# Performance work log

Measured on AMD Instinct MI355X. Metric: run time of the kernel, lower is better.

The kernel has to match this reference:

```python
import jax, jax.numpy as jnp
import numpy as np

B, N, D, C, NCLS = 8, 2048, 256, 128, 50
EPS = 1e-5  # BatchNorm eps

def _bn(x, g, b):
    # eval-mode BatchNorm1d over channel dim of (B,C,N): running_mean=0, running_var=1
    return x * (g / jnp.sqrt(1.0 + EPS))[:, None] + b[:, None]

def _complex_linear(x, Wr, br, Wi, bi):
    # torch ComplexLinear: complex(fr(x.real)-fi(x.imag), fr(x.imag)+fi(x.real))
    xr, xi = x.real, x.imag
    re = (xr @ Wr.T + br) - (xi @ Wi.T + bi)
    im = (xi @ Wr.T + br) + (xr @ Wi.T + bi)
    return jax.lax.complex(re, im)

def _sa(x, qkW, vW, vb, tW, tb, g, b):
    # x: (B,C,N); q/k share weights (tied in torch), dim C//4
    xq = jnp.einsum('qc,bcn->bnq', qkW, x)            # (B,N,C/4)
    xk = jnp.einsum('qc,bcm->bqm', qkW, x)            # (B,C/4,N)
    energy = jnp.einsum('bnq,bqm->bnm', xq, xk)       # (B,N,N)
    attn = jax.nn.softmax(energy, axis=-1)
    attn = attn / (1e-9 + attn.sum(axis=1, keepdims=True))  # column renorm
    xv = jnp.einsum('oc,bcn->bon', vW, x) + vb[:, None]
    xr = x - jnp.einsum('bcn,bnm->bcm', xv, attn)
    xr = jnp.einsum('oc,bcn->bon', tW, xr) + tb[:, None]
    return x + jax.nn.relu(_bn(xr, g, b))

def reference(xyz, cls_label, A, Bmat, W1r, b1r, W1i, b1i, W2r, b2r, W2i, b2i,
              lbl_emb, ft_w1, ft_g1, ft_b1, ft_w2, ft_g2, ft_b2,
              sa_qk, sa_vw, sa_vb, sa_tw, sa_tb, sa_g, sa_b,
              fuse_w, fuse_g, fuse_b, c1_w, c1_b, bn1_g, bn1_b, c2_w, c2_b):
    pts = xyz.transpose(0, 2, 1)                       # (B,N,3)
    # VecKM(d=256, alpha=30, beta=9): G = eB (eB^H eA), normalized to sqrt(d)
    eA = jnp.exp(1j * (pts @ A))                       # (B,N,D) complex64
    eB = jnp.exp(1j * (pts @ Bmat))
    inner = jnp.einsum('bnd,bne->bde', eB.conj(), eA)  # (B,D,D)
    G = jnp.einsum('bnd,bde->bne', eB, inner)          # (B,N,D)
    G = G / jnp.linalg.norm(G, axis=-1, keepdims=True) * jnp.sqrt(jnp.float32(D))
    G = _complex_linear(G, W1r, b1r, W1i, b1i)
    G = jax.lax.complex(jax.nn.relu(G.real), jax.nn.relu(G.imag))  # ComplexReLU
    G = _complex_linear(G, W2r, b2r, W2i, b2i)
    G = (G.real ** 2 + G.imag ** 2).transpose(0, 2, 1)  # (B,D,N)
    reweight = (cls_label @ lbl_emb)[:, :, None]        # (B,D,1)
    x = G * reweight
    x = jax.nn.relu(_bn(jnp.einsum('oc,bcn->bon', ft_w1, x), ft_g1, ft_b1))
    x = _bn(jnp.einsum('oc,bcn->bon', ft_w2, x), ft_g2, ft_b2)  # (B,C,N)
    feats = []
    for i in range(4):
        x = _sa(x, sa_qk[i], sa_vw[i], sa_vb[i], sa_tw[i], sa_tb[i], sa_g[i], sa_b[i])
        feats.append(x)
    x = jnp.concatenate(feats, axis=1)                  # (B,4C,N)
    x = jax.nn.relu(_bn(jnp.einsum('oc,bcn->bon', fuse_w, x), fuse_g, fuse_b))
    x = jax.nn.relu(_bn(jnp.einsum('oc,bcn->bon', c1_w, x) + c1_b[:, None], bn1_g, bn1_b))
    # dropout is identity in eval mode
    x = jnp.einsum('oc,bcn->bon', c2_w, x) + c2_b[:, None]
    x = jax.nn.log_softmax(x, axis=1)
    return x.transpose(0, 2, 1)                         # (B,N,NCLS)

def setup_inputs():
    key = jax.random.key(0)
    k = jax.random.split(key, 24)
    rn = lambda i, s: jax.random.normal(k[i], s, jnp.float32)
    s = 0.05
    return {
        'xyz': rn(0, (B, 3, N)),
        'cls_label': jax.random.uniform(k[1], (B, 16), jnp.float32),
        'A': rn(2, (3, D)) * 30.0,
        'Bmat': rn(3, (3, D)) * 9.0,
        'W1r': rn(4, (D, D)) * s, 'b1r': rn(5, (D,)) * s,
        'W1i': rn(6, (D, D)) * s, 'b1i': rn(7, (D,)) * s,
        'W2r': rn(8, (D, D)) * s, 'b2r': rn(9, (D,)) * s,
        'W2i': rn(10, (D, D)) * s, 'b2i': rn(11, (D,)) * s,
        'lbl_emb': rn(12, (16, D)),
        'ft_w1': rn(13, (C, D)) * s, 'ft_g1': jnp.ones((C,)), 'ft_b1': jnp.zeros((C,)),
        'ft_w2': rn(14, (C, C)) * s, 'ft_g2': jnp.ones((C,)), 'ft_b2': jnp.zeros((C,)),
        'sa_qk': rn(15, (4, C // 4, C)) * s,
        'sa_vw': rn(16, (4, C, C)) * s, 'sa_vb': rn(17, (4, C)) * s,
        'sa_tw': rn(18, (4, C, C)) * s, 'sa_tb': rn(19, (4, C)) * s,
        'sa_g': jnp.ones((4, C)), 'sa_b': jnp.zeros((4, C)),
        'fuse_w': rn(20, (C, 4 * C)) * s, 'fuse_g': jnp.ones((C,)), 'fuse_b': jnp.zeros((C,)),
        'c1_w': rn(21, (C, C)) * s, 'c1_b': rn(22, (C,)) * s,
        'bn1_g': jnp.ones((C,)), 'bn1_b': jnp.zeros((C,)),
        'c2_w': rn(23, (NCLS, C)) * s, 'c2_b': jnp.zeros((NCLS,)),
    }
```

## Files before the change

### kernel.cpp

```cpp
#include <hip/hip_runtime.h>

#define BB 8
#define NPTS 2048
#define DD 256
#define CCH 128
#define NCLASS 50
#define LOG2E 1.4426950408889634f

typedef __attribute__((ext_vector_type(8))) short short8;
typedef __attribute__((ext_vector_type(4))) float f32x4;
typedef unsigned short u16;
#define MFMA16(a,b,c) __builtin_amdgcn_mfma_f32_16x16x32_bf16(a,b,c,0,0,0)

__device__ __forceinline__ u16 f2bf(float x){
  union { float f; unsigned int u; } v; v.f = x;
  unsigned int r = v.u + 0x7FFFu + ((v.u >> 16) & 1u);
  return (u16)(r >> 16);
}
__device__ __forceinline__ float bf2f(u16 u){
  union { unsigned int u32; float f; } v; v.u32 = ((unsigned int)u) << 16; return v.f;
}
__device__ __forceinline__ void split2(float x, u16& h, u16& l){
  h = f2bf(x); l = f2bf(x - bf2f(h));
}
// ... 231 lines not shown
  for (int rg = 0; rg < 2; rg++) {
    ar_[rg] = (size_t)(m0 + wr + rg*16 + r16)*DD + g4*8;
    br_[rg] = (size_t)(o0 + wc + rg*16 + r16)*DD + g4*8;
  }
  #pragma unroll
  for (int k0 = 0; k0 < DD; k0 += 32) {
    short8 arh[2], arl[2], aih[2], ail[2], brh[2], brl[2], bih[2], bil[2];
    #pragma unroll
    for (int rg = 0; rg < 2; rg++) {
      arh[rg] = ld8(Arh + ar_[rg] + k0); arl[rg] = ld8(Arl + ar_[rg] + k0);
      aih[rg] = ld8(Aih + ar_[rg] + k0); ail[rg] = ld8(Ail + ar_[rg] + k0);
      brh[rg] = ld8(Wrh + br_[rg] + k0); brl[rg] = ld8(Wrl + br_[rg] + k0);
      bih[rg] = ld8(Wih + br_[rg] + k0); bil[rg] = ld8(Wil + br_[rg] + k0);
    }
    #pragma unroll
    for (int ra = 0; ra < 2; ra++)
      #pragma unroll
      for (int rb = 0; rb < 2; rb++) {
        p[ra][rb] = MFMA16(arh[ra], brh[rb], p[ra][rb]);
        p[ra][rb] = MFMA16(arh[ra], brl[rb], p[ra][rb]);
        p[ra][rb] = MFMA16(arl[ra], brh[rb], p[ra][rb]);
        q[ra][rb] = MFMA16(aih[ra], bih[rb], q[ra][rb]);
        q[ra][rb] = MFMA16(aih[ra], bil[rb], q[ra][rb]);
        q[ra][rb] = MFMA16(ail[ra], bih[rb], q[ra][rb]);
        im[ra][rb] = MFMA16(arh[ra], bih[rb], im[ra][rb]);
        im[ra][rb] = MFMA16(arh[ra], bil[rb], im[ra][rb]);
        im[ra][rb] = MFMA16(arl[ra], bih[rb], im[ra][rb]);
        im[ra][rb] = MFMA16(aih[ra], brh[rb], im[ra][rb]);
        im[ra][rb] = MFMA16(aih[ra], brl[rb], im[ra][rb]);
        im[ra][rb] = MFMA16(ail[ra], brh[rb], im[ra][rb]);
      }
  }
  #pragma unroll
  for (int ra = 0; ra < 2; ra++)
    #pragma unroll
    for (int rb = 0; rb < 2; rb++) {
      int o = o0 + wc + rb*16 + r16;
      float brv = br[o], biv = bi[o];
      if (mode == 1) {
        #pragma unroll
        for (int j = 0; j < 4; j++) {
          int m = m0 + wr + ra*16 + g4*4 + j;
          float re = fmaxf(p[ra][rb][j] - q[ra][rb][j] + brv - biv, 0.f);
          float iv = fmaxf(im[ra][rb][j] + brv + biv, 0.f);
          size_t off = (size_t)m*DD + o;
          u16 h, l;
          split2(re, h, l); Orh[off] = h; Orl[off] = l;
          split2(iv, h, l); Oih[off] = h; Oil[off] = l;
        }
      } else {
        int mbase = m0 + wr + ra*16 + g4*4;
        int b = mbase >> 11, nb = mbase & (NPTS-1);
        float rwv = RW[(size_t)b*DD + o];
        float4 gv;
        #pragma unroll
        for (int j = 0; j < 4; j++) {
          float re = p[ra][rb][j] - q[ra][rb][j] + brv - biv;
          float iv = im[ra][rb][j] + brv + biv;
          ((float*)&gv)[j] = (re*re + iv*iv) * rwv;
        }
        *(float4*)(GSQ + ((size_t)b*DD + o)*NPTS + nb) = gv;
      }
    }
}

__global__ void rw_kernel(const float* __restrict__ cls, const float* __restrict__ lbl,
                          float* __restrict__ RW)
{
  int b = blockIdx.x; int d = threadIdx.x;
  float s = 0.f;
  #pragma unroll
  for (int k = 0; k < 16; k++) s += cls[b*16+k] * lbl[k*DD+d];
  RW[b*DD+d] = s;
}

__global__ __launch_bounds__(256) void sgemm_kernel(
    const u16* __restrict__ Wh, const u16* __restrict__ Wl,
    const float* __restrict__ X, float* __restrict__ Y,
    const float* __restrict__ RES,
    const float* __restrict__ bias, const float* __restrict__ bng, const float* __restrict__ bnb,
    u16* __restrict__ YBh, u16* __restrict__ YBl, int ybmode,
    int O, int Cin, size_t xbs, size_t ybs, size_t rbs, int flags)
{
  int b = blockIdx.z;
  int n0 = blockIdx.x*64, o0 = blockIdx.y*64;
  const float* x = X + (size_t)b*xbs;
  __shared__ u16 sXh[64][40], sXl[64][40];
  int tid = threadIdx.x, lane = tid & 63, w = tid >> 6;
  int wo = (w >> 1)*32, wn = (w & 1)*32;
  int r16 = lane & 15, g4 = lane >> 4;
  f32x4 acc[2][2] = {};
  int stc = tid >> 3;
  int stn = (tid & 7)*8;
  for (int k0 = 0; k0 < Cin; k0 += 32) {
    const float* px = x + (size_t)(k0+stc)*NPTS + n0 + stn;
    float4 u0 = *(const float4*)px;
    float4 u1 = *(const float4*)(px+4);
    float v[8] = {u0.x,u0.y,u0.z,u0.w,u1.x,u1.y,u1.z,u1.w};
    __syncthreads();
    #pragma unroll
    for (int j = 0; j < 8; j++) {
      u16 h, l; split2(v[j], h, l);
      sXh[stn+j][stc] = h; sXl[stn+j][stc] = l;
    }
    __syncthreads();
    short8 awh[2], awl[2], bxh[2], bxl[2];
    #pragma unroll
    for (int rg = 0; rg < 2; rg++) {
      int orow = o0 + wo + rg*16 + r16;
      if (orow < O) {
        size_t woff = (size_t)orow*Cin + k0 + g4*8;
        awh[rg] = ld8(Wh + woff); awl[rg] = ld8(Wl + woff);
      } else { awh[rg] = zero8(); awl[rg] = zero8(); }
      bxh[rg] = ld8(&sXh[wn + rg*16 + r16][g4*8]);
      bxl[rg] = ld8(&sXl[wn + rg*16 + r16][g4*8]);
    }
    #pragma unroll
    for (int ra = 0; ra < 2; ra++)
      #pragma unroll
      for (int rb = 0; rb < 2; rb++) {
        acc[ra][rb] = MFMA16(awh[ra], bxh[rb], acc[ra][rb]);
        acc[ra][rb] = MFMA16(awh[ra], bxl[rb], acc[ra][rb]);
        acc[ra][rb] = MFMA16(awl[ra], bxh[rb], acc[ra][rb]);
      }
  }
  #pragma unroll
  for (int ra = 0; ra < 2; ra++)
    #pragma unroll
    for (int rb = 0; rb < 2; rb++)
      #pragma unroll
      for (int j = 0; j < 4; j++) {
        int o = o0 + wo + ra*16 + g4*4 + j;
        if (o >= O) continue;
        int n = n0 + wn + rb*16 + r16;
        float v = acc[ra][rb][j];
        if (flags & 1) v += bias[o];
        if (flags & 2) v = v * (bng[o] * rsqrtf(1.f + 1e-5f)) + bnb[o];
        if (flags & 4) v = fmaxf(v, 0.f);
        if (flags & 8) v += RES[(size_t)b*rbs + (size_t)o*NPTS + n];
        if (ybmode == 0) Y[(size_t)b*ybs + (size_t)o*NPTS + n] = v;
        else if (ybmode == 1) YBh[(size_t)b*ybs + (size_t)o*NPTS + n] = f2bf(v);
        else {
          u16 h, l; split2(v, h, l);
          size_t off = ((size_t)b*NPTS + n)*32 + o;
          YBh[off] = h; YBl[off] = l;
        }
      }
}

__global__ __launch_bounds__(256) void sastat_kernel(
    const u16* __restrict__ Qh, const u16* __restrict__ Ql,
    float* __restrict__ PM, float* __restrict__ PS)
{
  int b = blockIdx.z, ch = blockIdx.y;
  int n0 = blockIdx.x*64;
  size_t base = (size_t)b*NPTS*32;
  int tid = threadIdx.x, lane = tid & 63, wid = tid >> 6;
  int r16 = lane & 15, g4 = lane >> 4;
  size_t ao = base + (size_t)(n0 + wid*16 + r16)*32 + g4*8;
  short8 ah = ld8(Qh + ao), al = ld8(Ql + ao);
  float pm[4] = {-3.4e38f,-3.4e38f,-3.4e38f,-3.4e38f};
  float ps[4] = {0.f,0.f,0.f,0.f};
  int mbeg = ch*512, mend = mbeg + 512;
  for (int mt = mbeg; mt < mend; mt += 32) {
    size_t bo0 = base + (size_t)(mt + r16)*32 + g4*8;
    size_t bo1 = bo0 + 16*32;
    short8 bh0 = ld8(Qh+bo0), bl0 = ld8(Ql+bo0);
    short8 bh1 = ld8(Qh+bo1), bl1 = ld8(Ql+bo1);
    f32x4 a0 = {}, a1 = {};
    a0 = MFMA16(ah, bh0, a0); a0 = MFMA16(ah, bl0, a0); a0 = MFMA16(al, bh0, a0);
    a1 = MFMA16(ah, bh1, a1); a1 = MFMA16(ah, bl1, a1); a1 = MFMA16(al, bh1, a1);
    #pragma unroll
    for (int j = 0; j < 4; j++) {
      float v = fmaxf(a0[j], a1[j]);
      float mn = fmaxf(pm[j], v);
      ps[j] = ps[j]*exp2f((pm[j]-mn)*LOG2E)
            + exp2f((a0[j]-mn)*LOG2E) + exp2f((a1[j]-mn)*LOG2E);
      pm[j] = mn;
    }
  }
  #pragma unroll
  for (int j = 0; j < 4; j++) {
    float m = pm[j], s = ps[j];
    #pragma unroll
    for (int d = 1; d < 16; d <<= 1) {
      float om = __shfl_xor(m, d);
      float os = __shfl_xor(s, d);
      float mn = fmaxf(m, om);
      s = s*exp2f((m-mn)*LOG2E) + os*exp2f((om-mn)*LOG2E);
      m = mn;
    }
    if (r16 == 0) {
      int n_ = n0 + wid*16 + g4*4 + j;
      size_t off = ((size_t)ch*BB + b)*NPTS + n_;
      PM[off] = m; PS[off] = s;
    }
  }
}

__global__ __launch_bounds__(256) void comb1_kernel(
    const float* __restrict__ PM, const float* __restrict__ PS,
    float* __restrict__ MX, float* __restrict__ RS)
{
  size_t i = (size_t)blockIdx.x*256 + threadIdx.x;
  const size_t S = (size_t)BB*NPTS;
  float m0 = PM[i], m1 = PM[i+S], m2 = PM[i+2*S], m3 = PM[i+3*S];
  float mx = fmaxf(fmaxf(m0,m1), fmaxf(m2,m3));
  float den = PS[i]*exp2f((m0-mx)*LOG2E) + PS[i+S]*exp2f((m1-mx)*LOG2E)
            + PS[i+2*S]*exp2f((m2-mx)*LOG2E) + PS[i+3*S]*exp2f((m3-mx)*LOG2E);
  MX[i] = mx; RS[i] = 1.f/den;
}

__global__ __launch_bounds__(256) void fused_pv_kernel(
    const u16* __restrict__ Qh, const u16* __restrict__ Ql,
    const float* __restrict__ MX, const float* __restrict__ RS,
    const u16* __restrict__ XV, const float* __restrict__ XRES, size_t res_bs,
    float* __restrict__ OUT)
{
  int b = blockIdx.y;
  int m0 = blockIdx.x*16;
  size_t qbase = (size_t)b*NPTS*32;
  const u16* xv = XV + (size_t)b*CCH*NPTS;
  const float* mx = MX + (size_t)b*NPTS;
  const float* rs = RS + (size_t)b*NPTS;
  __shared__ u16 Pl[2][16][72];
  __shared__ float csacc[16];
  int tid = threadIdx.x, lane = tid & 63, w = tid >> 6;
  int r16 = lane & 15, g4 = lane >> 4;
  if (tid < 16) csacc[tid] = 0.f;
  int nb = w;
  int cw = w*32;
  int nloc = nb*16 + g4*4;
  size_t mo = qbase + (size_t)(m0 + r16)*32 + g4*8;
  short8 mbh = ld8(Qh + mo), mbl = ld8(Ql + mo);
  const u16* pa0 = xv + (size_t)(cw + r16)*NPTS + g4*8;
  const u16* pa1 = pa0 + (size_t)16*NPTS;
  f32x4 acc[2] = {};
  float csl = 0.f;

  #define COMPUTE_P(NT, BUF) { \
    size_t no_ = qbase + (size_t)((NT) + nb*16 + r16)*32 + g4*8; \
    short8 nah = ld8(Qh + no_), nal = ld8(Ql + no_); \
    f32x4 e = {}; \
    e = MFMA16(nah, mbh, e); e = MFMA16(nah, mbl, e); e = MFMA16(nal, mbh, e); \
    float4 mx4 = *(const float4*)&mx[(NT) + nloc]; \
    float4 rs4 = *(const float4*)&rs[(NT) + nloc]; \
    float t0 = exp2f((e[0]-mx4.x)*LOG2E)*rs4.x; \
    float t1 = exp2f((e[1]-mx4.y)*LOG2E)*rs4.y; \
    float t2 = exp2f((e[2]-mx4.z)*LOG2E)*rs4.z; \
    float t3 = exp2f((e[3]-mx4.w)*LOG2E)*rs4.w; \
    csl += t0 + t1 + t2 + t3; \
    uint2 pk; \
    pk.x = (unsigned)f2bf(t0) | ((unsigned)f2bf(t1) << 16); \
    pk.y = (unsigned)f2bf(t2) | ((unsigned)f2bf(t3) << 16); \
    *(uint2*)&Pl[BUF][r16][nloc] = pk; }

  COMPUTE_P(0, 0);
  __syncthreads();
  int cur = 0;
  for (int nt = 0; nt < NPTS; nt += 64) {
    short8 xa0 = ld8(pa0 + nt), xa1 = ld8(pa1 + nt);
    short8 xb0 = ld8(pa0 + nt + 32), xb1 = ld8(pa1 + nt + 32);
    short8 p0  = *(const short8*)&Pl[cur][r16][g4*8];
    short8 p0b = *(const short8*)&Pl[cur][r16][32 + g4*8];
    if (nt + 64 < NPTS) { COMPUTE_P(nt + 64, cur ^ 1); }
    acc[0] = MFMA16(xa0, p0, acc[0]);
    acc[1] = MFMA16(xa1, p0, acc[1]);
    acc[0] = MFMA16(xb0, p0b, acc[0]);
    acc[1] = MFMA16(xb1, p0b, acc[1]);
    __syncthreads();
    cur ^= 1;
  }
  #undef COMPUTE_P
  {
    float c = csl;
    c += __shfl_xor(c, 16);
    c += __shfl_xor(c, 32);
    if (g4 == 0) atomicAdd(&csacc[r16], c);
  }
  __syncthreads();
  float ci = 1.f/(1e-9f + csacc[r16]);
  int m = m0 + r16;
  #pragma unroll
  for (int ca = 0; ca < 2; ca++)
    #pragma unroll
    for (int j = 0; j < 4; j++) {
      int c = cw + ca*16 + g4*4 + j;
      float v = XRES[(size_t)b*res_bs + (size_t)c*NPTS + m] - acc[ca][j]*ci;
      OUT[((size_t)b*CCH + c)*NPTS + m] = v;
    }
}

__global__ __launch_bounds__(256) void lsm_kernel(const float* __restrict__ Y,
                                                  float* __restrict__ OUT)
{
  int idx = blockIdx.x*256 + threadIdx.x;
  int b = idx >> 11, n = idx & (NPTS-1);
  const float* p = Y + (size_t)b*NCLASS*NPTS + n;
  float m = -3.4e38f;
  #pragma unroll
  for (int k = 0; k < NCLASS; k++) m = fmaxf(m, p[(size_t)k*NPTS]);
  float s = 0.f;
  #pragma unroll
  for (int k = 0; k < NCLASS; k++) s += expf(p[(size_t)k*NPTS] - m);
  float L = m + logf(s);
  float* o = OUT + (size_t)idx*NCLASS;
  #pragma unroll
  for (int k = 0; k < NCLASS; k++) o[k] = p[(size_t)k*NPTS] - L;
}

extern "C" void kernel_launch(void* const* d_in, const int* in_sizes, int n_in,
                              void* d_out, int out_size, void* d_ws, size_t ws_size,
                              hipStream_t stream)
{
  (void)in_sizes; (void)n_in; (void)out_size; (void)ws_size;
  const float* xyz  = (const float*)d_in[0];
  const float* cls  = (const float*)d_in[1];
  const float* Amat = (const float*)d_in[2];
  const float* Bm   = (const float*)d_in[3];
  const float* W1r  = (const float*)d_in[4];
  const float* b1r  = (const float*)d_in[5];
  const float* W1i  = (const float*)d_in[6];
  const float* b1i  = (const float*)d_in[7];
  const float* W2r  = (const float*)d_in[8];
  const float* b2r  = (const float*)d_in[9];
  const float* W2i  = (const float*)d_in[10];
  const float* b2i  = (const float*)d_in[11];
  const float* lbl  = (const float*)d_in[12];
  const float* ftw1 = (const float*)d_in[13];
  const float* ftg1 = (const float*)d_in[14];
  const float* ftb1 = (const float*)d_in[15];
  const float* ftw2 = (const float*)d_in[16];
  const float* ftg2 = (const float*)d_in[17];
  const float* ftb2 = (const float*)d_in[18];
  const float* saqk = (const float*)d_in[19];
  const float* savw = (const float*)d_in[20];
  const float* savb = (const float*)d_in[21];
  const float* satw = (const float*)d_in[22];
  const float* satb = (const float*)d_in[23];
  const float* sag  = (const float*)d_in[24];
  const float* sab  = (const float*)d_in[25];
  const float* fusew= (const float*)d_in[26];
  const float* fuseg= (const float*)d_in[27];
  const float* fuseb= (const float*)d_in[28];
  const float* c1w  = (const float*)d_in[29];
  const float* c1b  = (const float*)d_in[30];
  const float* bn1g = (const float*)d_in[31];
  const float* bn1b = (const float*)d_in[32];
  const float* c2w  = (const float*)d_in[33];
  const float* c2b  = (const float*)d_in[34];
  float* out = (float*)d_out;

  float* ws = (float*)d_ws;
  const size_t PS  = (size_t)BB*DD*NPTS;
  const size_t ISZ = (size_t)BB*DD*DD;
  u16* U = (u16*)ws;
  u16 *ATrh = U+0*PS, *ATrl = U+1*PS, *ATih = U+2*PS, *ATil = U+3*PS;
  u16 *BTrh = U+4*PS, *BTrl = U+5*PS, *BTih = U+6*PS, *BTil = U+7*PS;
  u16 *Bnrh = U+8*PS, *Bnrl = U+9*PS, *Bnih = U+10*PS, *Bnil = U+11*PS;
  u16 *Irh = U+12*PS, *Irl = U+12*PS+ISZ, *Iih = U+12*PS+2*ISZ, *Iil = U+12*PS+3*ISZ;
  float* gsq = (float*)(U + 12*PS + 4*ISZ);
  float2* PART = (float2*)gsq;
  float2* Gf = (float2*)ws;
  u16 *G1rh = U+4*PS, *G1rl = U+5*PS, *G1ih = U+6*PS, *G1il = U+7*PS;
  u16 *G2rh = U+8*PS, *G2rl = U+9*PS, *G2ih = U+10*PS, *G2il = U+11*PS;
  size_t p = (size_t)BB*NPTS*NPTS;
  float* xfeat = ws + p;  p += (size_t)BB*CCH*NPTS;
  float* feats = ws + p;  p += (size_t)BB*4*CCH*NPTS;
  float* xt1   = ws + p;  p += (size_t)BB*CCH*NPTS;
  float* xt2   = ws + p;  p += (size_t)BB*CCH*NPTS;
  float* ybuf  = ws + p;  p += (size_t)BB*NCLASS*NPTS;
  float* rwb   = ws + p;  p += (size_t)BB*DD;
  float* mxv   = ws + p;  p += (size_t)BB*NPTS;
  float* rsv   = ws + p;  p += (size_t)BB*NPTS;
  float* PMb   = ws + p;  p += (size_t)4*BB*NPTS;
  float* PSb   = ws + p;  p += (size_t)4*BB*NPTS;
  u16* xqh = (u16*)(ws + p);
  u16* xql = xqh + (size_t)BB*NPTS*32;
  u16* xvb = xql + (size_t)BB*NPTS*32;
  u16* wpH = xvb + (size_t)BB*CCH*NPTS;
  u16* wpL = wpH + 557056;

  const int o_w1r=0, o_w1i=65536, o_w2r=131072, o_w2i=196608, o_ft1=262144,
            o_ft2=294912, o_qk=311296, o_vw=327680, o_tw=393216, o_fu=458752,
            o_c1=524288, o_c2=540672;
  WSplit wsp;
  const float* srcs[12] = {W1r,W1i,W2r,W2i,ftw1,ftw2,saqk,savw,satw,fusew,c1w,c2w};
  const int cnts[12] = {65536,65536,65536,65536,32768,16384,16384,65536,65536,65536,16384,6400};
  const int offs[12] = {o_w1r,o_w1i,o_w2r,o_w2i,o_ft1,o_ft2,o_qk,o_vw,o_tw,o_fu,o_c1,o_c2};
  for (int i = 0; i < 12; i++) { wsp.src[i]=srcs[i]; wsp.cnt[i]=cnts[i]; wsp.off[i]=offs[i]; }

  wsplit_kernel<<<dim3(256, 12), 256, 0, stream>>>(wsp, wpH, wpL);
  rw_kernel<<<BB, DD, 0, stream>>>(cls, lbl, rwb);
  ek1_kernel<<<(int)(PS/256), 256, 0, stream>>>(xyz, Amat, Bm,
      ATrh, ATrl, ATih, ATil, BTrh, BTrl, BTih, BTil);
  ek2_kernel<<<(int)(PS/256), 256, 0, stream>>>(xyz, Bm, Bnrh, Bnrl, Bnih, Bnil);
  inner_mfma_kernel<<<dim3(DD/64, DD/64, BB*4), 256, 0, stream>>>(
      ATrh, ATrl, ATih, ATil, BTrh, BTrl, BTih, BTil, PART);
  innred_kernel<<<(int)(ISZ/256), 256, 0, stream>>>(PART, Irh, Irl, Iih, Iil);
  g_mfma_kernel<<<dim3(DD/64, NPTS/64, BB), 256, 0, stream>>>(
      Bnrh, Bnrl, Bnih, Bnil, Irh, Irl, Iih, Iil, Gf);
  gnormsplit_kernel<<<BB*NPTS, 256, 0, stream>>>(Gf, G1rh, G1rl, G1ih, G1il);
  clinear_mfma_kernel<<<dim3(DD/64, (BB*NPTS)/64), 256, 0, stream>>>(
      G1rh, G1rl, G1ih, G1il, wpH+o_w1r, wpL+o_w1r, wpH+o_w1i, wpL+o_w1i,
      b1r, b1i, G2rh, G2rl, G2ih, G2il, nullptr, nullptr, 1);
  clinear_mfma_kernel<<<dim3(DD/64, (BB*NPTS)/64), 256, 0, stream>>>(
      G2rh, G2rl, G2ih, G2il, wpH+o_w2r, wpL+o_w2r, wpH+o_w2i, wpL+o_w2i,
      b2r, b2i, nullptr, nullptr, nullptr, nullptr, rwb, gsq, 2);

  sgemm_kernel<<<dim3(NPTS/64, CCH/64, BB), 256, 0, stream>>>(
      wpH+o_ft1, wpL+o_ft1, gsq, xt1, nullptr, nullptr, ftg1, ftb1, nullptr, nullptr, 0,
      CCH, DD, (size_t)DD*NPTS, (size_t)CCH*NPTS, 0, 2|4);
  sgemm_kernel<<<dim3(NPTS/64, CCH/64, BB), 256, 0, stream>>>(
      wpH+o_ft2, wpL+o_ft2, xt1, xfeat, nullptr, nullptr, ftg2, ftb2, nullptr, nullptr, 0,
      CCH, CCH, (size_t)CCH*NPTS, (size_t)CCH*NPTS, 0, 2);

  const float* xsrc = xfeat;
  size_t xbs = (size_t)CCH*NPTS;
  for (int i = 0; i < 4; i++) {
    sgemm_kernel<<<dim3(NPTS/64, 1, BB), 256, 0, stream>>>(
        wpH+o_qk + i*32*CCH, wpL+o_qk + i*32*CCH, xsrc, nullptr, nullptr,
        nullptr, nullptr, nullptr, xqh, xql, 2, 32, CCH, xbs, 0, 0, 0);
    sastat_kernel<<<dim3(NPTS/64, 4, BB), 256, 0, stream>>>(xqh, xql, PMb, PSb);
    comb1_kernel<<<(BB*NPTS)/256, 256, 0, stream>>>(PMb, PSb, mxv, rsv);
    sgemm_kernel<<<dim3(NPTS/64, CCH/64, BB), 256, 0, stream>>>(
        wpH+o_vw + i*CCH*CCH, wpL+o_vw + i*CCH*CCH, xsrc, nullptr, nullptr,
        savb + i*CCH, nullptr, nullptr, xvb, nullptr, 1, CCH, CCH, xbs,
        (size_t)CCH*NPTS, 0, 1);
    fused_pv_kernel<<<dim3(NPTS/16, BB), 256, 0, stream>>>(
        xqh, xql, mxv, rsv, xvb, xsrc, xbs, xt2);
    sgemm_kernel<<<dim3(NPTS/64, CCH/64, BB), 256, 0, stream>>>(
        wpH+o_tw + i*CCH*CCH, wpL+o_tw + i*CCH*CCH, xt2, feats + (size_t)i*CCH*NPTS, xsrc,
        satb + i*CCH, sag + i*CCH, sab + i*CCH, nullptr, nullptr, 0,
        CCH, CCH, (size_t)CCH*NPTS, (size_t)4*CCH*NPTS, xbs, 1|2|4|8);
    xsrc = feats + (size_t)i*CCH*NPTS;
    xbs = (size_t)4*CCH*NPTS;
  }

  sgemm_kernel<<<dim3(NPTS/64, CCH/64, BB), 256, 0, stream>>>(
      wpH+o_fu, wpL+o_fu, feats, xt1, nullptr, nullptr, fuseg, fuseb, nullptr, nullptr, 0,
      CCH, 4*CCH, (size_t)4*CCH*NPTS, (size_t)CCH*NPTS, 0, 2|4);
  sgemm_kernel<<<dim3(NPTS/64, CCH/64, BB), 256, 0, stream>>>(
      wpH+o_c1, wpL+o_c1, xt1, xt2, nullptr, c1b, bn1g, bn1b, nullptr, nullptr, 0,
      CCH, CCH, (size_t)CCH*NPTS, (size_t)CCH*NPTS, 0, 1|2|4);
  sgemm_kernel<<<dim3(NPTS/64, 1, BB), 256, 0, stream>>>(
      wpH+o_c2, wpL+o_c2, xt2, ybuf, nullptr, c2b, nullptr, nullptr, nullptr, nullptr, 0,
      NCLASS, CCH, (size_t)CCH*NPTS, (size_t)NCLASS*NPTS, 0, 1);
  lsm_kernel<<<(BB*NPTS)/256, 256, 0, stream>>>(ybuf, out);
}
```

Before: 997.1 us.

## Software-prefetch Q and XV loads and swizzle P tile in fused PV kernel

Register-prefetches the Q hi/lo fragments two tiles ahead and the XV fragments one tile ahead, so global load latency overlaps the MFMA and exp work of the current tile. It also replaces the padded shared-memory P buffer with an XOR-swizzled layout to avoid bank conflicts without padding. The cost is higher register pressure, which may reduce occupancy, plus extra index arithmetic.

```diff
diff --git a/kernel.cpp b/kernel.cpp
--- a/kernel.cpp
+++ b/kernel.cpp
@@ -478,26 +478,29 @@
   const u16* xv = XV + (size_t)b*CCH*NPTS;
   const float* mx = MX + (size_t)b*NPTS;
   const float* rs = RS + (size_t)b*NPTS;
-  __shared__ u16 Pl[2][16][72];
+  __shared__ u16 Pl[2][16*64];
   __shared__ float csacc[16];
   int tid = threadIdx.x, lane = tid & 63, w = tid >> 6;
   int r16 = lane & 15, g4 = lane >> 4;
   if (tid < 16) csacc[tid] = 0.f;
   int nb = w;
   int cw = w*32;
+  int swz = (r16 & 7) << 3;
   int nloc = nb*16 + g4*4;
+  int wrc = r16*64 + (nloc ^ swz);
+  int rd0 = r16*64 + ((g4*8) ^ swz);
+  int rd1 = r16*64 + ((32 + g4*8) ^ swz);
   size_t mo = qbase + (size_t)(m0 + r16)*32 + g4*8;
   short8 mbh = ld8(Qh + mo), mbl = ld8(Ql + mo);
   const u16* pa0 = xv + (size_t)(cw + r16)*NPTS + g4*8;
   const u16* pa1 = pa0 + (size_t)16*NPTS;
+  size_t q0 = qbase + (size_t)(nb*16 + r16)*32 + g4*8;
   f32x4 acc[2] = {};
   float csl = 0.f;
 
-  #define COMPUTE_P(NT, BUF) { \
-    size_t no_ = qbase + (size_t)((NT) + nb*16 + r16)*32 + g4*8; \
-    short8 nah = ld8(Qh + no_), nal = ld8(Ql + no_); \
+  #define COMPUTE_P(NT, QH, QL, BUF) { \
     f32x4 e = {}; \
-    e = MFMA16(nah, mbh, e); e = MFMA16(nah, mbl, e); e = MFMA16(nal, mbh, e); \
+    e = MFMA16(QH, mbh, e); e = MFMA16(QH, mbl, e); e = MFMA16(QL, mbh, e); \
     float4 mx4 = *(const float4*)&mx[(NT) + nloc]; \
     float4 rs4 = *(const float4*)&rs[(NT) + nloc]; \
     float t0 = exp2f((e[0]-mx4.x)*LOG2E)*rs4.x; \
@@ -508,22 +511,36 @@
     uint2 pk; \
     pk.x = (unsigned)f2bf(t0) | ((unsigned)f2bf(t1) << 16); \
     pk.y = (unsigned)f2bf(t2) | ((unsigned)f2bf(t3) << 16); \
-    *(uint2*)&Pl[BUF][r16][nloc] = pk; }
-
-  COMPUTE_P(0, 0);
+    *(uint2*)&Pl[BUF][wrc] = pk; }
+
+  short8 qh_c = ld8(Qh + q0), ql_c = ld8(Ql + q0);
+  short8 qh_n = ld8(Qh + q0 + (size_t)64*32), ql_n = ld8(Ql + q0 + (size_t)64*32);
+  short8 xa0 = ld8(pa0), xa1 = ld8(pa1);
+  short8 xb0 = ld8(pa0 + 32), xb1 = ld8(pa1 + 32);
+  COMPUTE_P(0, qh_c, ql_c, 0);
   __syncthreads();
   int cur = 0;
   for (int nt = 0; nt < NPTS; nt += 64) {
-    short8 xa0 = ld8(pa0 + nt), xa1 = ld8(pa1 + nt);
-    short8 xb0 = ld8(pa0 + nt + 32), xb1 = ld8(pa1 + nt + 32);
-    short8 p0  = *(const short8*)&Pl[cur][r16][g4*8];
-    short8 p0b = *(const short8*)&Pl[cur][r16][32 + g4*8];
-    if (nt + 64 < NPTS) { COMPUTE_P(nt + 64, cur ^ 1); }
+    short8 qh_2 = qh_n, ql_2 = ql_n;
+    short8 xn0 = xa0, xn1 = xa1, xn2 = xb0, xn3 = xb1;
+    if (nt + 128 < NPTS) {
+      size_t qo = q0 + (size_t)(nt + 128)*32;
+      qh_2 = ld8(Qh + qo); ql_2 = ld8(Ql + qo);
+    }
+    if (nt + 64 < NPTS) {
+      xn0 = ld8(pa0 + nt + 64); xn1 = ld8(pa1 + nt + 64);
+      xn2 = ld8(pa0 + nt + 96); xn3 = ld8(pa1 + nt + 96);
+    }
+    short8 p0  = ld8(&Pl[cur][rd0]);
+    short8 p0b = ld8(&Pl[cur][rd1]);
+    if (nt + 64 < NPTS) { COMPUTE_P(nt + 64, qh_n, ql_n, cur ^ 1); }
     acc[0] = MFMA16(xa0, p0, acc[0]);
     acc[1] = MFMA16(xa1, p0, acc[1]);
     acc[0] = MFMA16(xb0, p0b, acc[0]);
     acc[1] = MFMA16(xb1, p0b, acc[1]);
     __syncthreads();
+    qh_n = qh_2; ql_n = ql_2;
+    xa0 = xn0; xa1 = xn1; xb0 = xn2; xb1 = xn3;
     cur ^= 1;
   }
   #undef COMPUTE_P
```

Result: no change. 996.4 us (-0.1%).

## Enlarge fused attention-PV tile to 64 query columns with 8 waves and prefetch

Applied to the files above, without the earlier changes.

The fused softmax-times-V kernel now handles 64 output columns per block with 512 threads, where it previously handled 16 with 256. Each wave computes a 16x32 energy slab and reuses each loaded V fragment across four column sub-tiles, so V is read from global memory a quarter as often and the P tile is shared by more waves. The P tile in shared memory uses an XOR swizzle to avoid bank conflicts, and Q and V fragments are register-prefetched two iterations ahead. In exchange the kernel uses more registers and launches fewer blocks, which could lower occupancy.

```diff
diff --git a/kernel.cpp b/kernel.cpp
--- a/kernel.cpp
+++ b/kernel.cpp
@@ -466,64 +466,101 @@
   MX[i] = mx; RS[i] = 1.f/den;
 }
 
-__global__ __launch_bounds__(256) void fused_pv_kernel(
+__global__ __launch_bounds__(512) void fused_pv_kernel(
     const u16* __restrict__ Qh, const u16* __restrict__ Ql,
     const float* __restrict__ MX, const float* __restrict__ RS,
     const u16* __restrict__ XV, const float* __restrict__ XRES, size_t res_bs,
     float* __restrict__ OUT)
 {
   int b = blockIdx.y;
-  int m0 = blockIdx.x*16;
+  int m0 = blockIdx.x*64;
   size_t qbase = (size_t)b*NPTS*32;
   const u16* xv = XV + (size_t)b*CCH*NPTS;
   const float* mx = MX + (size_t)b*NPTS;
   const float* rs = RS + (size_t)b*NPTS;
-  __shared__ u16 Pl[2][16][72];
-  __shared__ float csacc[16];
+  __shared__ u16 Pl[2][64*66];
+  __shared__ float csacc[64];
   int tid = threadIdx.x, lane = tid & 63, w = tid >> 6;
   int r16 = lane & 15, g4 = lane >> 4;
-  if (tid < 16) csacc[tid] = 0.f;
-  int nb = w;
-  int cw = w*32;
-  int nloc = nb*16 + g4*4;
-  size_t mo = qbase + (size_t)(m0 + r16)*32 + g4*8;
+  if (tid < 64) csacc[tid] = 0.f;
+  int ma = w >> 1, na = w & 1;
+  int cw = w*16;
+  int swz = (r16 & 7) << 3;
+  size_t mo = qbase + (size_t)(m0 + ma*16 + r16)*32 + g4*8;
   short8 mbh = ld8(Qh + mo), mbl = ld8(Ql + mo);
-  const u16* pa0 = xv + (size_t)(cw + r16)*NPTS + g4*8;
-  const u16* pa1 = pa0 + (size_t)16*NPTS;
-  f32x4 acc[2] = {};
+  int wr_base = (ma*16 + r16)*66;
+  int nl0 = na*32 + g4*4;
+  const u16* pa = xv + (size_t)(cw + r16)*NPTS + g4*8;
+  size_t qn_off = qbase + (size_t)(na*32 + r16)*32 + g4*8;
+  f32x4 acc[4] = {};
   float csl = 0.f;
 
-  #define COMPUTE_P(NT, BUF) { \
-    size_t no_ = qbase + (size_t)((NT) + nb*16 + r16)*32 + g4*8; \
-    short8 nah = ld8(Qh + no_), nal = ld8(Ql + no_); \
-    f32x4 e = {}; \
-    e = MFMA16(nah, mbh, e); e = MFMA16(nah, mbl, e); e = MFMA16(nal, mbh, e); \
-    float4 mx4 = *(const float4*)&mx[(NT) + nloc]; \
-    float4 rs4 = *(const float4*)&rs[(NT) + nloc]; \
-    float t0 = exp2f((e[0]-mx4.x)*LOG2E)*rs4.x; \
-    float t1 = exp2f((e[1]-mx4.y)*LOG2E)*rs4.y; \
-    float t2 = exp2f((e[2]-mx4.z)*LOG2E)*rs4.z; \
-    float t3 = exp2f((e[3]-mx4.w)*LOG2E)*rs4.w; \
-    csl += t0 + t1 + t2 + t3; \
-    uint2 pk; \
-    pk.x = (unsigned)f2bf(t0) | ((unsigned)f2bf(t1) << 16); \
-    pk.y = (unsigned)f2bf(t2) | ((unsigned)f2bf(t3) << 16); \
-    *(uint2*)&Pl[BUF][r16][nloc] = pk; }
-
-  COMPUTE_P(0, 0);
+  #define COMPUTE_P(NT, QH0, QL0, QH1, QL1, BUF) { \
+    f32x4 e0 = {}, e1 = {}; \
+    e0 = MFMA16(QH0, mbh, e0); e0 = MFMA16(QH0, mbl, e0); e0 = MFMA16(QL0, mbh, e0); \
+    e1 = MFMA16(QH1, mbh, e1); e1 = MFMA16(QH1, mbl, e1); e1 = MFMA16(QL1, mbh, e1); \
+    { float4 m4 = *(const float4*)&mx[(NT) + nl0]; \
+      float4 r4 = *(const float4*)&rs[(NT) + nl0]; \
+      float t0 = exp2f((e0[0]-m4.x)*LOG2E)*r4.x; \
+      float t1 = exp2f((e0[1]-m4.y)*LOG2E)*r4.y; \
+      float t2 = exp2f((e0[2]-m4.z)*LOG2E)*r4.z; \
+      float t3 = exp2f((e0[3]-m4.w)*LOG2E)*r4.w; \
+      csl += t0 + t1 + t2 + t3; \
+      uint2 pk; \
+      pk.x = (unsigned)f2bf(t0) | ((unsigned)f2bf(t1) << 16); \
+      pk.y = (unsigned)f2bf(t2) | ((unsigned)f2bf(t3) << 16); \
+      *(uint2*)&Pl[BUF][wr_base + (nl0 ^ swz)] = pk; } \
+    { float4 m4 = *(const float4*)&mx[(NT) + nl0 + 16]; \
+      float4 r4 = *(const float4*)&rs[(NT) + nl0 + 16]; \
+      float t0 = exp2f((e1[0]-m4.x)*LOG2E)*r4.x; \
+      float t1 = exp2f((e1[1]-m4.y)*LOG2E)*r4.y; \
+      float t2 = exp2f((e1[2]-m4.z)*LOG2E)*r4.z; \
+      float t3 = exp2f((e1[3]-m4.w)*LOG2E)*r4.w; \
+      csl += t0 + t1 + t2 + t3; \
+      uint2 pk; \
+      pk.x = (unsigned)f2bf(t0) | ((unsigned)f2bf(t1) << 16); \
+      pk.y = (unsigned)f2bf(t2) | ((unsigned)f2bf(t3) << 16); \
+      *(uint2*)&Pl[BUF][wr_base + ((nl0 + 16) ^ swz)] = pk; } }
+
+  short8 qch[2], qcl[2], qnh[2], qnl[2];
+  #pragma unroll
+  for (int s = 0; s < 2; s++) {
+    size_t o = qn_off + (size_t)(s*16)*32;
+    qch[s] = ld8(Qh + o); qcl[s] = ld8(Ql + o);
+    o += (size_t)64*32;
+    qnh[s] = ld8(Qh + o); qnl[s] = ld8(Ql + o);
+  }
+  short8 xa0 = ld8(pa), xa1 = ld8(pa + 32);
+  short8 xn0 = ld8(pa + 64), xn1 = ld8(pa + 96);
+  COMPUTE_P(0, qch[0], qcl[0], qch[1], qcl[1], 0);
   __syncthreads();
   int cur = 0;
   for (int nt = 0; nt < NPTS; nt += 64) {
-    short8 xa0 = ld8(pa0 + nt), xa1 = ld8(pa1 + nt);
-    short8 xb0 = ld8(pa0 + nt + 32), xb1 = ld8(pa1 + nt + 32);
-    short8 p0  = *(const short8*)&Pl[cur][r16][g4*8];
-    short8 p0b = *(const short8*)&Pl[cur][r16][32 + g4*8];
-    if (nt + 64 < NPTS) { COMPUTE_P(nt + 64, cur ^ 1); }
-    acc[0] = MFMA16(xa0, p0, acc[0]);
-    acc[1] = MFMA16(xa1, p0, acc[1]);
-    acc[0] = MFMA16(xb0, p0b, acc[0]);
-    acc[1] = MFMA16(xb1, p0b, acc[1]);
+    short8 q2h[2], q2l[2], x20, x21;
+    if (nt + 128 < NPTS) {
+      #pragma unroll
+      for (int s = 0; s < 2; s++) {
+        size_t o = qn_off + (size_t)(nt + 128 + s*16)*32;
+        q2h[s] = ld8(Qh + o); q2l[s] = ld8(Ql + o);
+      }
+      x20 = ld8(pa + nt + 128); x21 = ld8(pa + nt + 160);
+    } else { q2h[0]=q2h[1]=q2l[0]=q2l[1]=x20=x21=zero8(); }
+    short8 pf0[4], pf1[4];
+    #pragma unroll
+    for (int mf = 0; mf < 4; mf++) {
+      int rowb = (mf*16 + r16)*66;
+      pf0[mf] = ld8(&Pl[cur][rowb + ((g4*8) ^ swz)]);
+      pf1[mf] = ld8(&Pl[cur][rowb + ((32 + g4*8) ^ swz)]);
+    }
+    if (nt + 64 < NPTS) { COMPUTE_P(nt + 64, qnh[0], qnl[0], qnh[1], qnl[1], cur ^ 1); }
+    #pragma unroll
+    for (int mf = 0; mf < 4; mf++) {
+      acc[mf] = MFMA16(xa0, pf0[mf], acc[mf]);
+      acc[mf] = MFMA16(xa1, pf1[mf], acc[mf]);
+    }
     __syncthreads();
+    qnh[0]=q2h[0]; qnh[1]=q2h[1]; qnl[0]=q2l[0]; qnl[1]=q2l[1];
+    xa0 = xn0; xa1 = xn1; xn0 = x20; xn1 = x21;
     cur ^= 1;
   }
   #undef COMPUTE_P
@@ -531,19 +568,20 @@
     float c = csl;
     c += __shfl_xor(c, 16);
     c += __shfl_xor(c, 32);
-    if (g4 == 0) atomicAdd(&csacc[r16], c);
+    if (g4 == 0) atomicAdd(&csacc[ma*16 + r16], c);
   }
   __syncthreads();
-  float ci = 1.f/(1e-9f + csacc[r16]);
-  int m = m0 + r16;
-  #pragma unroll
-  for (int ca = 0; ca < 2; ca++)
+  #pragma unroll
+  for (int mf = 0; mf < 4; mf++) {
+    int m = m0 + mf*16 + r16;
+    float ci = 1.f/(1e-9f + csacc[mf*16 + r16]);
     #pragma unroll
     for (int j = 0; j < 4; j++) {
-      int c = cw + ca*16 + g4*4 + j;
-      float v = XRES[(size_t)b*res_bs + (size_t)c*NPTS + m] - acc[ca][j]*ci;
+      int c = cw + g4*4 + j;
+      float v = XRES[(size_t)b*res_bs + (size_t)c*NPTS + m] - acc[mf][j]*ci;
       OUT[((size_t)b*CCH + c)*NPTS + m] = v;
     }
+  }
 }
 
 __global__ __launch_bounds__(256) void lsm_kernel(const float* __restrict__ Y,
@@ -682,7 +720,7 @@
         wpH+o_vw + i*CCH*CCH, wpL+o_vw + i*CCH*CCH, xsrc, nullptr, nullptr,
         savb + i*CCH, nullptr, nullptr, xvb, nullptr, 1, CCH, CCH, xbs,
         (size_t)CCH*NPTS, 0, 1);
-    fused_pv_kernel<<<dim3(NPTS/16, BB), 256, 0, stream>>>(
+    fused_pv_kernel<<<dim3(NPTS/64, BB), 512, 0, stream>>>(
         xqh, xql, mxv, rsv, xvb, xsrc, xbs, xt2);
     sgemm_kernel<<<dim3(NPTS/64, CCH/64, BB), 256, 0, stream>>>(
         wpH+o_tw + i*CCH*CCH, wpL+o_tw + i*CCH*CCH, xt2, feats + (size_t)i*CCH*NPTS, xsrc,
```

After: 962.2 us. 1.04x faster.

## Split attention PV over key chunks with per-wave register P and combine kernel

Applied to the files above, without the earlier changes.

Rewrites the fused attention-times-value kernel so each wave owns 16 query columns and one quarter of the key range. The P tile is redistributed through lane shuffles instead of a double-buffered LDS tile, which removes the per-iteration block barrier. Partial accumulators and column sums are written to workspace and reduced by a new sacomb kernel that applies the renormalisation and residual through an LDS transpose. Block indices in both attention kernels are linearised with batch innermost. This buys more parallelism and no barriers at the cost of extra global traffic for partials and one more launch.

```diff
diff --git a/kernel.cpp b/kernel.cpp
--- a/kernel.cpp
+++ b/kernel.cpp
@@ -407,8 +407,11 @@
     const u16* __restrict__ Qh, const u16* __restrict__ Ql,
     float* __restrict__ PM, float* __restrict__ PS)
 {
-  int b = blockIdx.z, ch = blockIdx.y;
-  int n0 = blockIdx.x*64;
+  int bx = blockIdx.x;
+  int b = bx & 7;
+  int t = bx >> 3;
+  int ch = t & 3;
+  int n0 = (t >> 2)*64;
   size_t base = (size_t)b*NPTS*32;
   int tid = threadIdx.x, lane = tid & 63, wid = tid >> 6;
   int r16 = lane & 15, g4 = lane >> 4;
@@ -469,81 +472,126 @@
 __global__ __launch_bounds__(256) void fused_pv_kernel(
     const u16* __restrict__ Qh, const u16* __restrict__ Ql,
     const float* __restrict__ MX, const float* __restrict__ RS,
-    const u16* __restrict__ XV, const float* __restrict__ XRES, size_t res_bs,
-    float* __restrict__ OUT)
-{
-  int b = blockIdx.y;
-  int m0 = blockIdx.x*16;
+    const u16* __restrict__ XV,
+    float* __restrict__ ACCp, float* __restrict__ CSPp)
+{
+  int bx = blockIdx.x;
+  int b = bx & 7;
+  int r = bx >> 3;
+  int ch = r & 3;
+  int mtile = r >> 2;
+  int tid = threadIdx.x, lane = tid & 63, w = tid >> 6;
+  int r16 = lane & 15, g4 = lane >> 4;
+  int m0w = mtile*64 + w*16;
   size_t qbase = (size_t)b*NPTS*32;
   const u16* xv = XV + (size_t)b*CCH*NPTS;
   const float* mx = MX + (size_t)b*NPTS;
   const float* rs = RS + (size_t)b*NPTS;
-  __shared__ u16 Pl[2][16][72];
-  __shared__ float csacc[16];
-  int tid = threadIdx.x, lane = tid & 63, w = tid >> 6;
-  int r16 = lane & 15, g4 = lane >> 4;
-  if (tid < 16) csacc[tid] = 0.f;
-  int nb = w;
-  int cw = w*32;
-  int nloc = nb*16 + g4*4;
-  size_t mo = qbase + (size_t)(m0 + r16)*32 + g4*8;
+  size_t mo = qbase + (size_t)(m0w + r16)*32 + g4*8;
   short8 mbh = ld8(Qh + mo), mbl = ld8(Ql + mo);
-  const u16* pa0 = xv + (size_t)(cw + r16)*NPTS + g4*8;
-  const u16* pa1 = pa0 + (size_t)16*NPTS;
-  f32x4 acc[2] = {};
+  f32x4 acc[8] = {};
   float csl = 0.f;
-
-  #define COMPUTE_P(NT, BUF) { \
-    size_t no_ = qbase + (size_t)((NT) + nb*16 + r16)*32 + g4*8; \
-    short8 nah = ld8(Qh + no_), nal = ld8(Ql + no_); \
-    f32x4 e = {}; \
-    e = MFMA16(nah, mbh, e); e = MFMA16(nah, mbl, e); e = MFMA16(nal, mbh, e); \
-    float4 mx4 = *(const float4*)&mx[(NT) + nloc]; \
-    float4 rs4 = *(const float4*)&rs[(NT) + nloc]; \
-    float t0 = exp2f((e[0]-mx4.x)*LOG2E)*rs4.x; \
-    float t1 = exp2f((e[1]-mx4.y)*LOG2E)*rs4.y; \
-    float t2 = exp2f((e[2]-mx4.z)*LOG2E)*rs4.z; \
-    float t3 = exp2f((e[3]-mx4.w)*LOG2E)*rs4.w; \
-    csl += t0 + t1 + t2 + t3; \
-    uint2 pk; \
-    pk.x = (unsigned)f2bf(t0) | ((unsigned)f2bf(t1) << 16); \
-    pk.y = (unsigned)f2bf(t2) | ((unsigned)f2bf(t3) << 16); \
-    *(uint2*)&Pl[BUF][r16][nloc] = pk; }
-
-  COMPUTE_P(0, 0);
+  int nbeg = ch*512;
+  int sq = (g4 & 1)*32 + r16;
+  const u16* pb_base = xv + (size_t)r16*NPTS + g4*8;
+  for (int it = 0; it < 16; it++) {
+    int nt = nbeg + it*32;
+    f32x4 e0 = {}, e1 = {};
+    {
+      size_t no = qbase + (size_t)(nt + r16)*32 + g4*8;
+      short8 nh = ld8(Qh + no), nl = ld8(Ql + no);
+      e0 = MFMA16(nh, mbh, e0); e0 = MFMA16(nh, mbl, e0); e0 = MFMA16(nl, mbh, e0);
+      no += (size_t)16*32;
+      short8 nh1 = ld8(Qh + no), nl1 = ld8(Ql + no);
+      e1 = MFMA16(nh1, mbh, e1); e1 = MFMA16(nh1, mbl, e1); e1 = MFMA16(nl1, mbh, e1);
+    }
+    unsigned pk00, pk01, pk10, pk11;
+    {
+      float4 m4 = *(const float4*)&mx[nt + 4*g4];
+      float4 r4 = *(const float4*)&rs[nt + 4*g4];
+      float t0 = exp2f((e0[0]-m4.x)*LOG2E)*r4.x;
+      float t1 = exp2f((e0[1]-m4.y)*LOG2E)*r4.y;
+      float t2 = exp2f((e0[2]-m4.z)*LOG2E)*r4.z;
+      float t3 = exp2f((e0[3]-m4.w)*LOG2E)*r4.w;
+      csl += t0+t1+t2+t3;
+      pk00 = (unsigned)f2bf(t0) | ((unsigned)f2bf(t1)<<16);
+      pk01 = (unsigned)f2bf(t2) | ((unsigned)f2bf(t3)<<16);
+      m4 = *(const float4*)&mx[nt + 16 + 4*g4];
+      r4 = *(const float4*)&rs[nt + 16 + 4*g4];
+      t0 = exp2f((e1[0]-m4.x)*LOG2E)*r4.x;
+      t1 = exp2f((e1[1]-m4.y)*LOG2E)*r4.y;
+      t2 = exp2f((e1[2]-m4.z)*LOG2E)*r4.z;
+      t3 = exp2f((e1[3]-m4.w)*LOG2E)*r4.w;
+      csl += t0+t1+t2+t3;
+      pk10 = (unsigned)f2bf(t0) | ((unsigned)f2bf(t1)<<16);
+      pk11 = (unsigned)f2bf(t2) | ((unsigned)f2bf(t3)<<16);
+    }
+    int a00 = __shfl((int)pk00, sq);
+    int a01 = __shfl((int)pk01, sq);
+    int a10 = __shfl((int)pk10, sq);
+    int a11 = __shfl((int)pk11, sq);
+    int b00 = __shfl((int)pk00, sq+16);
+    int b01 = __shfl((int)pk01, sq+16);
+    int b10 = __shfl((int)pk10, sq+16);
+    int b11 = __shfl((int)pk11, sq+16);
+    bool lo = (lane < 32);
+    union { int u[4]; short8 s; } af;
+    af.u[0] = lo ? a00 : a10;
+    af.u[1] = lo ? a01 : a11;
+    af.u[2] = lo ? b00 : b10;
+    af.u[3] = lo ? b01 : b11;
+    const u16* pb = pb_base + nt;
+    #pragma unroll
+    for (int ct = 0; ct < 8; ct++) {
+      short8 bf = ld8(pb + (size_t)(ct*16)*NPTS);
+      acc[ct] = MFMA16(af.s, bf, acc[ct]);
+    }
+  }
+  csl += __shfl_xor(csl, 16);
+  csl += __shfl_xor(csl, 32);
+  size_t pbase = (size_t)(ch*BB + b);
+  if (lane < 16) CSPp[pbase*NPTS + m0w + r16] = csl;
+  #pragma unroll
+  for (int ct = 0; ct < 8; ct++)
+    #pragma unroll
+    for (int j = 0; j < 4; j++)
+      ACCp[(pbase*NPTS + (size_t)(m0w + 4*g4 + j))*CCH + ct*16 + r16] = acc[ct][j];
+}
+
+__global__ __launch_bounds__(256) void sacomb_kernel(
+    const float* __restrict__ ACCp, const float* __restrict__ CSPp,
+    const float* __restrict__ XRES, size_t res_bs, float* __restrict__ OUT)
+{
+  int mt = blockIdx.x;
+  int b = blockIdx.y;
+  int m0 = mt*64;
+  __shared__ float T[128][65];
+  __shared__ float cinv[64];
+  int tid = threadIdx.x;
+  const size_t S = (size_t)BB*NPTS;
+  if (tid < 64) {
+    size_t o = (size_t)b*NPTS + m0 + tid;
+    float c = CSPp[o] + CSPp[S+o] + CSPp[2*S+o] + CSPp[3*S+o];
+    cinv[tid] = 1.f/(1e-9f + c);
+  }
   __syncthreads();
-  int cur = 0;
-  for (int nt = 0; nt < NPTS; nt += 64) {
-    short8 xa0 = ld8(pa0 + nt), xa1 = ld8(pa1 + nt);
-    short8 xb0 = ld8(pa0 + nt + 32), xb1 = ld8(pa1 + nt + 32);
-    short8 p0  = *(const short8*)&Pl[cur][r16][g4*8];
-    short8 p0b = *(const short8*)&Pl[cur][r16][32 + g4*8];
-    if (nt + 64 < NPTS) { COMPUTE_P(nt + 64, cur ^ 1); }
-    acc[0] = MFMA16(xa0, p0, acc[0]);
-    acc[1] = MFMA16(xa1, p0, acc[1]);
-    acc[0] = MFMA16(xb0, p0b, acc[0]);
-    acc[1] = MFMA16(xb1, p0b, acc[1]);
-    __syncthreads();
-    cur ^= 1;
-  }
-  #undef COMPUTE_P
   {
-    float c = csl;
-    c += __shfl_xor(c, 16);
-    c += __shfl_xor(c, 32);
-    if (g4 == 0) atomicAdd(&csacc[r16], c);
+    int c = tid & 127, mh = tid >> 7;
+    const size_t SA = (size_t)BB*NPTS*CCH;
+    for (int ml = mh; ml < 64; ml += 2) {
+      size_t o = ((size_t)b*NPTS + m0 + ml)*CCH + c;
+      float s = ACCp[o] + ACCp[SA+o] + ACCp[2*SA+o] + ACCp[3*SA+o];
+      T[c][ml] = s * cinv[ml];
+    }
   }
   __syncthreads();
-  float ci = 1.f/(1e-9f + csacc[r16]);
-  int m = m0 + r16;
-  #pragma unroll
-  for (int ca = 0; ca < 2; ca++)
-    #pragma unroll
-    for (int j = 0; j < 4; j++) {
-      int c = cw + ca*16 + g4*4 + j;
-      float v = XRES[(size_t)b*res_bs + (size_t)c*NPTS + m] - acc[ca][j]*ci;
-      OUT[((size_t)b*CCH + c)*NPTS + m] = v;
-    }
+  {
+    int m = tid & 63, c4 = tid >> 6;
+    for (int cl = c4; cl < 128; cl += 4) {
+      size_t o = (size_t)b*res_bs + (size_t)cl*NPTS + m0 + m;
+      OUT[((size_t)b*CCH + cl)*NPTS + m0 + m] = XRES[o] - T[cl][m];
+    }
+  }
 }
 
 __global__ __launch_bounds__(256) void lsm_kernel(const float* __restrict__ Y,
@@ -619,6 +667,8 @@
   float2* Gf = (float2*)ws;
   u16 *G1rh = U+4*PS, *G1rl = U+5*PS, *G1ih = U+6*PS, *G1il = U+7*PS;
   u16 *G2rh = U+8*PS, *G2rl = U+9*PS, *G2ih = U+10*PS, *G2il = U+11*PS;
+  float* ACCp = ws;
+  float* CSPp = ws + (size_t)4*BB*NPTS*CCH;
   size_t p = (size_t)BB*NPTS*NPTS;
   float* xfeat = ws + p;  p += (size_t)BB*CCH*NPTS;
   float* feats = ws + p;  p += (size_t)BB*4*CCH*NPTS;
@@ -676,14 +726,16 @@
     sgemm_kernel<<<dim3(NPTS/64, 1, BB), 256, 0, stream>>>(
         wpH+o_qk + i*32*CCH, wpL+o_qk + i*32*CCH, xsrc, nullptr, nullptr,
         nullptr, nullptr, nullptr, xqh, xql, 2, 32, CCH, xbs, 0, 0, 0);
-    sastat_kernel<<<dim3(NPTS/64, 4, BB), 256, 0, stream>>>(xqh, xql, PMb, PSb);
+    sastat_kernel<<<1024, 256, 0, stream>>>(xqh, xql, PMb, PSb);
     comb1_kernel<<<(BB*NPTS)/256, 256, 0, stream>>>(PMb, PSb, mxv, rsv);
     sgemm_kernel<<<dim3(NPTS/64, CCH/64, BB), 256, 0, stream>>>(
         wpH+o_vw + i*CCH*CCH, wpL+o_vw + i*CCH*CCH, xsrc, nullptr, nullptr,
         savb + i*CCH, nullptr, nullptr, xvb, nullptr, 1, CCH, CCH, xbs,
         (size_t)CCH*NPTS, 0, 1);
-    fused_pv_kernel<<<dim3(NPTS/16, BB), 256, 0, stream>>>(
-        xqh, xql, mxv, rsv, xvb, xsrc, xbs, xt2);
+    fused_pv_kernel<<<1024, 256, 0, stream>>>(
+        xqh, xql, mxv, rsv, xvb, ACCp, CSPp);
+    sacomb_kernel<<<dim3(NPTS/64, BB), 256, 0, stream>>>(
+        ACCp, CSPp, xsrc, xbs, xt2);
     sgemm_kernel<<<dim3(NPTS/64, CCH/64, BB), 256, 0, stream>>>(
         wpH+o_tw + i*CCH*CCH, wpL+o_tw + i*CCH*CCH, xt2, feats + (size_t)i*CCH*NPTS, xsrc,
         satb + i*CCH, sag + i*CCH, sab + i*CCH, nullptr, nullptr, 0,
```

After: 1.037 ms. 1.04x slower.
